# Optimization experiments

Hardware: AMD Instinct MI355X
Metric: run time of the kernel (lower is better)

Reference implementation:

```python
import jax, jax.numpy as jnp
import numpy as np

B, COND_LEN, E = 128, 256, 512   # batch, cond_len, hidden_dim (== conditioning_dim)
A, L, H = 128, 64, 8             # action_dim, num_action_steps, num_heads
STEPS = 20
HD = E // H


def setup_inputs() -> dict:
    key = jax.random.key(0)
    ks = jax.random.split(key, 16)
    def rn(k, shape, s=0.02):
        return jax.random.normal(k, shape, jnp.float32) * s
    return {
        "conditioning": jax.random.normal(ks[0], (B, COND_LEN, E), jnp.float32),
        "noise": jax.random.normal(ks[1], (B, L, A), jnp.float32),
        # time_embed: Linear(1,E) -> ReLU -> Linear(E,E)
        "t1_w": rn(ks[2], (E, 1)), "t1_b": jnp.zeros((E,), jnp.float32),
        "t2_w": rn(ks[3], (E, E)), "t2_b": jnp.zeros((E,), jnp.float32),
        # query_proj: Linear(A, E)
        "qp_w": rn(ks[4], (E, A)), "qp_b": jnp.zeros((E,), jnp.float32),
        # MultiheadAttention packed in_proj (3E, E) and out_proj (E, E)
        "in_w": rn(ks[5], (3 * E, E)), "in_b": jnp.zeros((3 * E,), jnp.float32),
        "op_w": rn(ks[6], (E, E)), "op_b": jnp.zeros((E,), jnp.float32),
        # output_proj: Linear(E, A)
        "outp_w": rn(ks[7], (A, E)), "outp_b": jnp.zeros((A,), jnp.float32),
        # ffn: Linear(A, 4A) -> ReLU -> Linear(4A, A)
        "f1_w": rn(ks[8], (4 * A, A)), "f1_b": jnp.zeros((4 * A,), jnp.float32),
        "f2_w": rn(ks[9], (A, 4 * A)), "f2_b": jnp.zeros((A,), jnp.float32),
        # LayerNorm(A)
        "ln_g": jnp.ones((A,), jnp.float32), "ln_b": jnp.zeros((A,), jnp.float32),
    }


def reference(conditioning, noise, t1_w, t1_b, t2_w, t2_b, qp_w, qp_b,
              in_w, in_b, op_w, op_b, outp_w, outp_b,
              f1_w, f1_b, f2_w, f2_b, ln_g, ln_b):
    dt = -1.0 / STEPS
    scale = 1.0 / np.sqrt(HD)
    # K/V of cross-attn depend only on conditioning -> hoist out of the loop
    # (same math as recomputing per step).
    k = (conditioning @ in_w[E:2 * E].T + in_b[E:2 * E]).reshape(B, COND_LEN, H, HD)
    v = (conditioning @ in_w[2 * E:].T + in_b[2 * E:]).reshape(B, COND_LEN, H, HD)

    def denoise(x_t, time):
        t = time[:, None]                                            # (B,1)
        t_emb = jnp.maximum(t @ t1_w.T + t1_b, 0.0) @ t2_w.T + t2_b  # (B,E)
        q_in = x_t @ qp_w.T + qp_b + t_emb[:, None, :]               # (B,L,E)
        q = (q_in @ in_w[:E].T + in_b[:E]).reshape(B, L, H, HD)
        scores = jnp.einsum('bqhd,bkhd->bhqk', q * scale, k)         # (B,H,L,COND_LEN)
        attn = jax.nn.softmax(scores, axis=-1)
        ctx = jnp.einsum('bhqk,bkhd->bqhd', attn, v).reshape(B, L, E)
        ctx = ctx @ op_w.T + op_b                                    # MHA out_proj
        v_t = ctx @ outp_w.T + outp_b                                # (B,L,A)
        h = x_t + v_t
        mu = jnp.mean(h, axis=-1, keepdims=True)
        var = jnp.mean((h - mu) ** 2, axis=-1, keepdims=True)
        hn = (h - mu) / jnp.sqrt(var + 1e-5) * ln_g + ln_b
        return hn + (jnp.maximum(hn @ f1_w.T + f1_b, 0.0) @ f2_w.T + f2_b)

    def step(carry, _):
        x_t, time = carry
        v_t = denoise(x_t, time)
        return (x_t + dt * v_t, time + dt), None

    init = (noise, jnp.ones((B,), jnp.float32))
    (x_t, _), _ = jax.lax.scan(step, init, None, length=STEPS)
    return x_t
```

## Files before the change

### kernel.cpp

```cpp
#include <hip/hip_runtime.h>

#define NB 128
#define CL 256
#define EE 512
#define AA 128
#define LL 64
#define HH 8
#define HD 64
#define NSTEPS 20
#define BLROWS (NB*LL)
#define LOG2E 1.4426950408889634f
#define QSCALE 64.0f
#define INV_QS 0.015625f

typedef __attribute__((ext_vector_type(8))) short bf16x8;
typedef __attribute__((ext_vector_type(4))) float f32x4;
typedef unsigned int u32;

union F8 { u32 u[2]; long l; };

__device__ __forceinline__ unsigned short f2bf(float f) {
    union { float f; unsigned u; } x; x.f = f;
    unsigned u = x.u;
    u += 0x7fffu + ((u >> 16) & 1u);
    return (unsigned short)(u >> 16);
}
__device__ __forceinline__ u32 pk4f8(f32x4 v) {
    u32 r = __builtin_amdgcn_cvt_pk_fp8_f32(v[0], v[1], 0, false);
    r = __builtin_amdgcn_cvt_pk_fp8_f32(v[2], v[3], r, true);
    return r;
}
__device__ __forceinline__ unsigned char f2f8(float v) {
    return (unsigned char)(__builtin_amdgcn_cvt_pk_fp8_f32(v, v, 0, false) & 0xffu);
}

__device__ __forceinline__ void async_copy16(const unsigned short* g, unsigned short* l) {
    __builtin_amdgcn_global_load_lds((const __attribute__((address_space(1))) u32*)g,
                                     (__attribute__((address_space(3))) u32*)l, 16, 0, 0);
}

#define MFMA(a,b,c)  __builtin_amdgcn_mfma_f32_16x16x32_bf16(a, b, c, 0, 0, 0)
#define MFMA8(a,b,c) __builtin_amdgcn_mfma_f32_16x16x32_fp8_fp8(a, b, c, 0, 0, 0)

__device__ __forceinline__ F8 build8(const u32* p, int kk, int srcA, int srcB, int odd) {
    u32 a0 = __shfl((int)p[2*kk],   srcA, 64);
    u32 b0 = __shfl((int)p[2*kk+1], srcA, 64);
    u32 a1 = __shfl((int)p[2*kk],   srcB, 64);
    u32 b1 = __shfl((int)p[2*kk+1], srcB, 64);
    F8 f; f.u[0] = odd ? b0 : a0; f.u[1] = odd ? b1 : a1;
    return f;
}

__device__ __forceinline__ float softmax8v(const f32x4* sacc, u32* pp8) {
    float mx0 = sacc[0][0], mx1 = sacc[0][1], mx2 = sacc[0][2], mx3 = sacc[0][3];
#pragma unroll
    for (int t = 1; t < 16; ++t) {
        mx0 = fmaxf(mx0, sacc[t][0]);
        mx1 = fmaxf(mx1, sacc[t][1]);
        mx2 = fmaxf(mx2, sacc[t][2]);
        mx3 = fmaxf(mx3, sacc[t][3]);
    }
    float mx = fmaxf(fmaxf(mx0, mx1), fmaxf(mx2, mx3));
    mx = fmaxf(mx, __shfl_xor(mx, 16));
    mx = fmaxf(mx, __shfl_xor(mx, 32));
    float mxc = mx * INV_QS;
    float s0 = 0.f, s1 = 0.f, s2 = 0.f, s3 = 0.f;
#pragma unroll
    for (int t = 0; t < 16; ++t) {
        float e0 = exp2f(fmaf(sacc[t][0], INV_QS, -mxc));
        float e1 = exp2f(fmaf(sacc[t][1], INV_QS, -mxc));
        float e2 = exp2f(fmaf(sacc[t][2], INV_QS, -mxc));
        float e3 = exp2f(fmaf(sacc[t][3], INV_QS, -mxc));
        s0 += e0; s1 += e1; s2 += e2; s3 += e3;
        f32x4 w;
        w[0] = e0 * QSCALE; w[1] = e1 * QSCALE;
        w[2] = e2 * QSCALE; w[3] = e3 * QSCALE;
        pp8[t] = pk4f8(w);
    }
    float sum = (s0 + s1) + (s2 + s3);
    sum += __shfl_xor(sum, 16);
    sum += __shfl_xor(sum, 32);
    return 1.0f / sum;
}


__global__ void cvt8_kernel(const float* __restrict__ src, unsigned short* __restrict__ dst, int n8) {
    int i = blockIdx.x*256 + threadIdx.x;
    if (i >= n8) return;
    const float* s = src + (size_t)i*8;
    f32x4 v0 = *(const f32x4*)s;
    f32x4 v1 = *(const f32x4*)(s + 4);
    bf16x8 o;
    o[0]=(short)f2bf(v0[0]); o[1]=(short)f2bf(v0[1]);
    o[2]=(short)f2bf(v0[2]); o[3]=(short)f2bf(v0[3]);
    o[4]=(short)f2bf(v1[0]); o[5]=(short)f2bf(v1[1]);
    o[6]=(short)f2bf(v1[2]); o[7]=(short)f2bf(v1[3]);
    *(bf16x8*)(dst + (size_t)i*8) = o;
}

__global__ void prep_eff_kernel(const float* __restrict__ in_w, const float* __restrict__ qp_w,
                                const float* __restrict__ outp_w, const float* __restrict__ op_w,
                                const float* __restrict__ op_b, const float* __restrict__ outp_b,
                                unsigned short* __restrict__ wq, unsigned short* __restrict__ wo,
                                float* __restrict__ bo) {
    int tid = blockIdx.x*256 + threadIdx.x;
    if (tid < 65536) {
        int n = tid >> 7, k = tid & 127;
        float s = 0.f;
        for (int e = 0; e < 512; ++e) s += in_w[(size_t)n*512 + e] * qp_w[(size_t)e*128 + k];
        wq[(size_t)n*128 + k] = f2bf(s * (0.125f * LOG2E * QSCALE));
    } else if (tid < 131072) {
        int t2 = tid - 65536; int n = t2 >> 9, k = t2 & 511;
        float s = 0.f;
        for (int e = 0; e < 512; ++e) s += outp_w[(size_t)n*512 + e] * op_w[(size_t)e*512 + k];
        wo[(size_t)n*512 + k] = f2bf(s);
    } else if (tid < 131200) {
        int n = tid - 131072;
        float s = outp_b[n];
        for (int e = 0; e < 512; ++e) s += outp_w[(size_t)n*512 + e] * op_b[e];
        bo[n] = s;
    }
}

__global__ void temb_kernel(const float* __restrict__ t1_w, const float* __restrict__ t1_b,
                            const float* __restrict__ t2_w, const float* __restrict__ t2_b,
                            float* __restrict__ temb) {
    int tid = blockIdx.x*256 + threadIdx.x;
    if (tid >= NSTEPS*512) return;
    int s = tid >> 9, e = tid & 511;
    float t = 1.0f - 0.05f * (float)s;
    float acc = t2_b[e];
    for (int i = 0; i < 512; ++i)
        acc += t2_w[(size_t)e*512 + i] * fmaxf(t * t1_w[i] + t1_b[i], 0.f);
    temb[tid] = acc;
}

__global__ void qbias_kernel(const float* __restrict__ in_w, const float* __restrict__ in_b,
                             const float* __restrict__ qp_b, const float* __restrict__ temb,
                             float* __restrict__ qbias) {
    int tid = blockIdx.x*256 + threadIdx.x;
    if (tid >= NSTEPS*512) return;
    int s = tid >> 9, n = tid & 511;
    float acc = in_b[n];
    const float* te = temb + (size_t)s*512;
    for (int e = 0; e < 512; ++e)
        acc += in_w[(size_t)n*512 + e] * (qp_b[e] + te[e]);
    qbias[tid] = acc * (0.125f * LOG2E * QSCALE);
}

__global__ __launch_bounds__(512, 8) void kv_kernel(const unsigned short* __restrict__ condb,
                                                    const unsigned short* __restrict__ wkv,
                                                    const float* __restrict__ bias,
                                                    unsigned char* __restrict__ K8,
                                                    unsigned char* __restrict__ V8) {
    __shared__ unsigned short As[128*64];
    __shared__ unsigned short Bs[128*64];
    int tid = threadIdx.x;
    int blk = blockIdx.x;
    int xcd = blk & 7, j = blk >> 3;
    int m0 = (xcd*32 + (j >> 3)) * 128;
    int n0 = (j & 7) * 128;
    int wv = tid >> 6, lane = tid & 63, r = lane & 15, q = lane >> 4;
    int srow = lane >> 3;
    int sg = (lane & 7) ^ srow;
    const unsigned short* agl = condb + (size_t)(m0 + wv*16 + srow)*512 + sg*8;
    const unsigned short* bgl = wkv   + (size_t)(n0 + wv*16 + srow)*512 + sg*8;
    f32x4 acc[8] = {};
#pragma unroll
    for (int kt = 0; kt < 8; ++kt) {
        int k0 = kt * 64;
#pragma unroll
        for (int ii = 0; ii < 2; ++ii) {
            async_copy16(agl + (size_t)(ii*8)*512 + k0, &As[(wv*16 + ii*8)*64]);
            async_copy16(bgl + (size_t)(ii*8)*512 + k0, &Bs[(wv*16 + ii*8)*64]);
        }
        __syncthreads();
#pragma unroll
        for (int kk = 0; kk < 2; ++kk) {
            int gof = ((kk*4 + q) ^ (r & 7)) * 8;
            bf16x8 a = *(const bf16x8*)&As[(wv*16 + r)*64 + gof];
#pragma unroll
            for (int t = 0; t < 8; ++t) {
                bf16x8 b = *(const bf16x8*)&Bs[(t*16 + r)*64 + gof];
                acc[t] = MFMA(a, b, acc[t]);
            }
        }
        __syncthreads();
    }
    int mbase = m0 + wv*16 + q*4;
    int bb = mbase >> 8, kpb = mbase & 255;
#pragma unroll
    for (int t = 0; t < 8; ++t) {
        int n = n0 + t*16 + r;
        float bs = bias[n];
        if (n < 512) {
            int h = n >> 6, d = n & 63;
            int colp = ((d>>3)&3)*16 + ((d>>5)&1)*8 + (d&7);
            unsigned char* kp = K8 + (size_t)(bb*HH + h)*16384 + colp;
#pragma unroll
            for (int i = 0; i < 4; ++i)
                kp[(kpb + i)*64] = f2f8(acc[t][i] + bs);
        } else {
            int n2 = n - 512, h = n2 >> 6, d = n2 & 63;
            int kk = kpb >> 5, qq = (kpb >> 3) & 3, jb = kpb & 7;
            int colv = (kk>>1)*64 + qq*16 + (kk&1)*8 + jb;
            u32 w01 = __builtin_amdgcn_cvt_pk_fp8_f32(acc[t][0]+bs, acc[t][1]+bs, 0, false);
            w01 = __builtin_amdgcn_cvt_pk_fp8_f32(acc[t][2]+bs, acc[t][3]+bs, w01, true);
            *(u32*)(V8 + (size_t)(bb*HH + h)*16384 + d*256 + colv) = w01;
        }
    }
}

__global__ __launch_bounds__(512, 2) void mega_kernel(
        const unsigned char* __restrict__ Kg,
        const unsigned char* __restrict__ Vg,
        const float* __restrict__ noise,
        const unsigned short* __restrict__ wq,
        const float* __restrict__ qbiasB,
        const unsigned short* __restrict__ wo,
        const float* __restrict__ bo,
        const float* __restrict__ ln_g, const float* __restrict__ ln_b,
        const unsigned short* __restrict__ f1w,
        const float* __restrict__ f1_b,
        const unsigned short* __restrict__ f2w,
        const float* __restrict__ f2_b,
        float* __restrict__ outp) {
    __shared__ unsigned short xS[32*136];
    __shared__ unsigned short cuS[32*520];
    __shared__ unsigned short hnS[32*136];
    __shared__ float redS[32*4], redS2[32*4];

    int tid = threadIdx.x, w = tid >> 6, lane = tid & 63, r = lane & 15, q = lane >> 4;
    int vblk = ((blockIdx.x & 7) << 5) | (blockIdx.x >> 3);
    int b = vblk >> 1;
    int row0 = vblk * 32;
    int h = w;
    int tB = w & 1, cg = w >> 1;
    int srcA = r + ((2*q) & 3)*16;
    int srcB = r + ((2*q + 1) & 3)*16;
    int odd = (q >> 1) & 1;

    float xf[2][4];
#pragma unroll
    for (int t = 0; t < 2; ++t)
#pragma unroll
        for (int i = 0; i < 4; ++i) {
            int rl = tB*16 + q*4 + i, col = cg*32 + t*16 + r;
            float v = noise[(size_t)(row0 + rl)*AA + col];
            xf[t][i] = v;
            xS[rl*136 + col] = f2bf(v);
        }

    size_t bh = (size_t)b*HH + h;
    const unsigned char* kbase = Kg + bh*16384;
    const unsigned char* vbase = Vg + bh*16384;
    __syncthreads();

    const float dt = -1.f / (float)NSTEPS;

#pragma unroll 1
    for (int s = 0; s < NSTEPS; ++s) {
        const float* qb_s = qbiasB + (size_t)s*512;

        {
            uint4 kbuf[16];
#pragma unroll
            for (int t = 0; t < 16; ++t)
                kbuf[t] = *(const uint4*)(kbase + (size_t)(t*16 + r)*64 + q*16);

            f32x4 qacc0[4] = {}, qacc1[4] = {};
#pragma unroll
            for (int kk = 0; kk < 4; ++kk) {
                bf16x8 bx0 = *(const bf16x8*)&xS[(r)*136 + kk*32 + q*8];
                bf16x8 bx1 = *(const bf16x8*)&xS[(16 + r)*136 + kk*32 + q*8];
#pragma unroll
                for (int t = 0; t < 4; ++t) {
                    bf16x8 a = *(const bf16x8*)(wq + (size_t)(h*HD + t*16 + r)*AA + kk*32 + q*8);
                    qacc0[t] = MFMA(a, bx0, qacc0[t]);
                    qacc1[t] = MFMA(a, bx1, qacc1[t]);
                }
            }
            u32 qp0[4], qp1[4];
#pragma unroll
            for (int t = 0; t < 4; ++t) {
                f32x4 qb4 = *(const f32x4*)(qb_s + h*HD + t*16 + q*4);
                f32x4 v0, v1;
#pragma unroll
                for (int i = 0; i < 4; ++i) { v0[i] = qacc0[t][i] + qb4[i]; v1[i] = qacc1[t][i] + qb4[i]; }
                qp0[t] = pk4f8(v0);
                qp1[t] = pk4f8(v1);
            }
            F8 bq0[2], bq1[2];
            bq0[0] = build8(qp0, 0, srcA, srcB, odd);
            bq0[1] = build8(qp0, 1, srcA, srcB, odd);
            bq1[0] = build8(qp1, 0, srcA, srcB, odd);
            bq1[1] = build8(qp1, 1, srcA, srcB, odd);

            f32x4 s0[16] = {}, s1[16] = {};
#pragma unroll
            for (int t = 0; t < 16; ++t) {
                F8 k0, k1;
                k0.u[0] = kbuf[t].x; k0.u[1] = kbuf[t].y;
                k1.u[0] = kbuf[t].z; k1.u[1] = kbuf[t].w;
                s0[t] = MFMA8(k0.l, bq0[0].l, s0[t]);
                s0[t] = MFMA8(k1.l, bq0[1].l, s0[t]);
                s1[t] = MFMA8(k0.l, bq1[0].l, s1[t]);
                s1[t] = MFMA8(k1.l, bq1[1].l, s1[t]);
            }

            uint4 vbuf[16];
#pragma unroll
            for (int kp = 0; kp < 4; ++kp)
#pragma unroll
                for (int t = 0; t < 4; ++t)
                    vbuf[kp*4 + t] = *(const uint4*)(vbase + (size_t)(t*16 + r)*256 + kp*64 + q*16);

            u32 pp0[16], pp1[16];
            float iv0 = softmax8v(s0, pp0);
            float iv1 = softmax8v(s1, pp1);

            f32x4 c0[4] = {}, c1[4] = {};
#pragma unroll
            for (int kp = 0; kp < 4; ++kp) {
                F8 a00 = build8(pp0, 2*kp,   srcA, srcB, odd);
                F8 a01 = build8(pp0, 2*kp+1, srcA, srcB, odd);
                F8 a10 = build8(pp1, 2*kp,   srcA, srcB, odd);
                F8 a11 = build8(pp1, 2*kp+1, srcA, srcB, odd);
#pragma unroll
                for (int t = 0; t < 4; ++t) {
                    F8 v0, v1;
                    v0.u[0] = vbuf[kp*4+t].x; v0.u[1] = vbuf[kp*4+t].y;
                    v1.u[0] = vbuf[kp*4+t].z; v1.u[1] = vbuf[kp*4+t].w;
                    c0[t] = MFMA8(a00.l, v0.l, c0[t]);
                    c0[t] = MFMA8(a01.l, v1.l, c0[t]);
                    c1[t] = MFMA8(a10.l, v0.l, c1[t]);
                    c1[t] = MFMA8(a11.l, v1.l, c1[t]);
                }
            }
            float sc0[4], sc1[4];
#pragma unroll
            for (int i = 0; i < 4; ++i) {
                sc0[i] = INV_QS * __shfl(iv0, q*4 + i);
                sc1[i] = INV_QS * __shfl(iv1, q*4 + i);
            }
#pragma unroll
            for (int t = 0; t < 4; ++t)
#pragma unroll
                for (int i = 0; i < 4; ++i) {
                    cuS[(q*4 + i)*520 + h*HD + t*16 + r]      = f2bf(c0[t][i] * sc0[i]);
                    cuS[(16 + q*4 + i)*520 + h*HD + t*16 + r] = f2bf(c1[t][i] * sc1[i]);
                }
        }
        __syncthreads();

        f32x4 oacc[2] = {};
#pragma unroll
        for (int kk = 0; kk < 16; ++kk) {
            bf16x8 a = *(const bf16x8*)&cuS[(tB*16 + r)*520 + kk*32 + q*8];
#pragma unroll
            for (int t = 0; t < 2; ++t) {
                bf16x8 bw = *(const bf16x8*)(wo + (size_t)(cg*32 + t*16 + r)*EE + kk*32 + q*8);
                oacc[t] = MFMA(a, bw, oacc[t]);
            }
        }
        float hv[2][4];
#pragma unroll
        for (int t = 0; t < 2; ++t) {
            float bov = bo[cg*32 + t*16 + r];
#pragma unroll
            for (int i = 0; i < 4; ++i) hv[t][i] = oacc[t][i] + bov + xf[t][i];
        }
#pragma unroll
        for (int i = 0; i < 4; ++i) {
            float s1 = hv[0][i] + hv[1][i];
            float s2 = hv[0][i]*hv[0][i] + hv[1][i]*hv[1][i];
            s1 += __shfl_xor(s1, 1);  s2 += __shfl_xor(s2, 1);
            s1 += __shfl_xor(s1, 2);  s2 += __shfl_xor(s2, 2);
            s1 += __shfl_xor(s1, 4);  s2 += __shfl_xor(s2, 4);
            s1 += __shfl_xor(s1, 8);  s2 += __shfl_xor(s2, 8);
            if (r == 0) { redS[(tB*16 + q*4 + i)*4 + cg] = s1; redS2[(tB*16 + q*4 + i)*4 + cg] = s2; }
        }
        __syncthreads();
        float hnv[2][4];
#pragma unroll
        for (int i = 0; i < 4; ++i) {
            int row = tB*16 + q*4 + i;
            float s1 = redS [row*4+0] + redS [row*4+1] + redS [row*4+2] + redS [row*4+3];
            float s2 = redS2[row*4+0] + redS2[row*4+1] + redS2[row*4+2] + redS2[row*4+3];
            float mu = s1 * (1.f/128.f);
            float var = s2 * (1.f/128.f) - mu*mu;
            float rstd = rsqrtf(var + 1e-5f);
#pragma unroll
            for (int t = 0; t < 2; ++t) {
                int col = cg*32 + t*16 + r;
                float v = (hv[t][i] - mu) * rstd * ln_g[col] + ln_b[col];
                hnv[t][i] = v;
                hnS[row*136 + col] = f2bf(v);
            }
        }
        __syncthreads();

        f32x4 o2[2] = {};
#pragma unroll 1
        for (int nt = 0; nt < 4; ++nt) {
            f32x4 a1[2] = {};
#pragma unroll
            for (int kk = 0; kk < 4; ++kk) {
                bf16x8 a = *(const bf16x8*)&hnS[(tB*16 + r)*136 + kk*32 + q*8];
#pragma unroll
                for (int t = 0; t < 2; ++t) {
                    bf16x8 bw = *(const bf16x8*)(f1w + (size_t)(nt*128 + cg*32 + t*16 + r)*AA + kk*32 + q*8);
                    a1[t] = MFMA(a, bw, a1[t]);
                }
            }
#pragma unroll
            for (int t = 0; t < 2; ++t) {
                float b1 = f1_b[nt*128 + cg*32 + t*16 + r];
#pragma unroll
                for (int i = 0; i < 4; ++i)
                    cuS[(tB*16 + q*4 + i)*520 + nt*128 + cg*32 + t*16 + r] = f2bf(fmaxf(a1[t][i] + b1, 0.f));
            }
        }
        __syncthreads();
#pragma unroll 1
        for (int nt = 0; nt < 4; ++nt) {
#pragma unroll
            for (int kk = 0; kk < 4; ++kk) {
                bf16x8 a = *(const bf16x8*)&cuS[(tB*16 + r)*520 + nt*128 + kk*32 + q*8];
#pragma unroll
                for (int t = 0; t < 2; ++t) {
                    bf16x8 bw = *(const bf16x8*)(f2w + (size_t)(cg*32 + t*16 + r)*EE + nt*128 + kk*32 + q*8);
                    o2[t] = MFMA(a, bw, o2[t]);
                }
            }
        }

        if (s < NSTEPS - 1) {
#pragma unroll
            for (int t = 0; t < 2; ++t) {
                float b2 = f2_b[cg*32 + t*16 + r];
#pragma unroll
                for (int i = 0; i < 4; ++i) {
                    float outv = hnv[t][i] + o2[t][i] + b2;
                    float xn = xf[t][i] + dt * outv;
                    xf[t][i] = xn;
                    xS[(tB*16 + q*4 + i)*136 + cg*32 + t*16 + r] = f2bf(xn);
                }
            }
            __syncthreads();
        } else {
#pragma unroll
            for (int t = 0; t < 2; ++t) {
                float b2 = f2_b[cg*32 + t*16 + r];
#pragma unroll
                for (int i = 0; i < 4; ++i) {
                    float outv = hnv[t][i] + o2[t][i] + b2;
                    outp[(size_t)(row0 + tB*16 + q*4 + i)*AA + cg*32 + t*16 + r] = xf[t][i] + dt * outv;
                }
            }
        }
    }
}

extern "C" void kernel_launch(void* const* d_in, const int* in_sizes, int n_in,
                              void* d_out, int out_size, void* d_ws, size_t ws_size,
                              hipStream_t stream) {
    const float* cond   = (const float*)d_in[0];
    const float* noise  = (const float*)d_in[1];
    const float* t1_w   = (const float*)d_in[2];
    const float* t1_b   = (const float*)d_in[3];
    const float* t2_w   = (const float*)d_in[4];
    const float* t2_b   = (const float*)d_in[5];
    const float* qp_w   = (const float*)d_in[6];
    const float* qp_b   = (const float*)d_in[7];
    const float* in_w   = (const float*)d_in[8];
    const float* in_b   = (const float*)d_in[9];
    const float* op_w   = (const float*)d_in[10];
    const float* op_b   = (const float*)d_in[11];
    const float* outp_w = (const float*)d_in[12];
    const float* outp_b = (const float*)d_in[13];
    const float* f1_w   = (const float*)d_in[14];
    const float* f1_b   = (const float*)d_in[15];
    const float* f2_w   = (const float*)d_in[16];
    const float* f2_b   = (const float*)d_in[17];
    const float* ln_g   = (const float*)d_in[18];
    const float* ln_bp  = (const float*)d_in[19];

    char* w = (char*)d_ws;
    auto alloc = [&](size_t bytes) {
        char* p = w;
        w += (bytes + 255) & ~(size_t)255;
        return p;
    };
    unsigned char*  K8     = (unsigned char*)alloc((size_t)NB*HH*CL*HD);
    unsigned char*  V8     = (unsigned char*)alloc((size_t)NB*HH*HD*CL);
    unsigned short* condb  = (unsigned short*)alloc((size_t)NB*CL*EE*2);
    unsigned short* wkv_bf = (unsigned short*)alloc((size_t)1024*512*2);
    unsigned short* wq_bf  = (unsigned short*)alloc((size_t)512*128*2);
    unsigned short* wo_bf  = (unsigned short*)alloc((size_t)128*512*2);
    unsigned short* f1_bf  = (unsigned short*)alloc((size_t)512*128*2);
    unsigned short* f2_bf  = (unsigned short*)alloc((size_t)128*512*2);
    float*          bo_eff = (float*)alloc(128*4);
    float*          tembB  = (float*)alloc((size_t)NSTEPS*512*4);
    float*          qbiasB = (float*)alloc((size_t)NSTEPS*512*4);
    (void)ws_size; (void)n_in; (void)in_sizes; (void)out_size;

    cvt8_kernel<<<8192, 256, 0, stream>>>(cond, condb, NB*CL*EE/8);
    cvt8_kernel<<<256, 256, 0, stream>>>(in_w + 512*512, wkv_bf, 1024*512/8);
    cvt8_kernel<<<32, 256, 0, stream>>>(f1_w, f1_bf, 512*128/8);
    cvt8_kernel<<<32, 256, 0, stream>>>(f2_w, f2_bf, 128*512/8);
    prep_eff_kernel<<<513, 256, 0, stream>>>(in_w, qp_w, outp_w, op_w, op_b, outp_b,
                                             wq_bf, wo_bf, bo_eff);
    temb_kernel<<<40, 256, 0, stream>>>(t1_w, t1_b, t2_w, t2_b, tembB);
    qbias_kernel<<<40, 256, 0, stream>>>(in_w, in_b, qp_b, tembB, qbiasB);
    kv_kernel<<<2048, 512, 0, stream>>>(condb, wkv_bf, in_b + 512, K8, V8);

    mega_kernel<<<256, 512, 0, stream>>>(K8, V8, noise, wq_bf, qbiasB,
                                         wo_bf, bo_eff, ln_g, ln_bp,
                                         f1_bf, f1_b, f2_bf, f2_b,
                                         (float*)d_out);
}
```

Before: 1.369 ms.

## Split attention over key halves with online softmax to cut register pressure

Replaces the single-pass softmax over all 256 keys with a two-chunk online-softmax (flash-style) loop, loading half of K and V per chunk. Running max and sum are rescaled between chunks and the context accumulators are rescaled before each chunk's PV MFMAs. The aim is to halve the live K/V buffers and score accumulators, easing VGPR pressure and possibly raising occupancy or avoiding spills. In exchange it adds rescaling exps, shuffles and multiplies, and puts a serial dependency between the two chunks.

```diff
diff --git a/kernel.cpp b/kernel.cpp
--- a/kernel.cpp
+++ b/kernel.cpp
@@ -49,38 +49,6 @@
     u32 b1 = __shfl((int)p[2*kk+1], srcB, 64);
     F8 f; f.u[0] = odd ? b0 : a0; f.u[1] = odd ? b1 : a1;
     return f;
-}
-
-__device__ __forceinline__ float softmax8v(const f32x4* sacc, u32* pp8) {
-    float mx0 = sacc[0][0], mx1 = sacc[0][1], mx2 = sacc[0][2], mx3 = sacc[0][3];
-#pragma unroll
-    for (int t = 1; t < 16; ++t) {
-        mx0 = fmaxf(mx0, sacc[t][0]);
-        mx1 = fmaxf(mx1, sacc[t][1]);
-        mx2 = fmaxf(mx2, sacc[t][2]);
-        mx3 = fmaxf(mx3, sacc[t][3]);
-    }
-    float mx = fmaxf(fmaxf(mx0, mx1), fmaxf(mx2, mx3));
-    mx = fmaxf(mx, __shfl_xor(mx, 16));
-    mx = fmaxf(mx, __shfl_xor(mx, 32));
-    float mxc = mx * INV_QS;
-    float s0 = 0.f, s1 = 0.f, s2 = 0.f, s3 = 0.f;
-#pragma unroll
-    for (int t = 0; t < 16; ++t) {
-        float e0 = exp2f(fmaf(sacc[t][0], INV_QS, -mxc));
-        float e1 = exp2f(fmaf(sacc[t][1], INV_QS, -mxc));
-        float e2 = exp2f(fmaf(sacc[t][2], INV_QS, -mxc));
-        float e3 = exp2f(fmaf(sacc[t][3], INV_QS, -mxc));
-        s0 += e0; s1 += e1; s2 += e2; s3 += e3;
-        f32x4 w;
-        w[0] = e0 * QSCALE; w[1] = e1 * QSCALE;
-        w[2] = e2 * QSCALE; w[3] = e3 * QSCALE;
-        pp8[t] = pk4f8(w);
-    }
-    float sum = (s0 + s1) + (s2 + s3);
-    sum += __shfl_xor(sum, 16);
-    sum += __shfl_xor(sum, 32);
-    return 1.0f / sum;
 }
 
 
@@ -263,11 +231,6 @@
         const float* qb_s = qbiasB + (size_t)s*512;
 
         {
-            uint4 kbuf[16];
-#pragma unroll
-            for (int t = 0; t < 16; ++t)
-                kbuf[t] = *(const uint4*)(kbase + (size_t)(t*16 + r)*64 + q*16);
-
             f32x4 qacc0[4] = {}, qacc1[4] = {};
 #pragma unroll
             for (int kk = 0; kk < 4; ++kk) {
@@ -296,47 +259,115 @@
             bq1[0] = build8(qp1, 0, srcA, srcB, odd);
             bq1[1] = build8(qp1, 1, srcA, srcB, odd);
 
-            f32x4 s0[16] = {}, s1[16] = {};
-#pragma unroll
-            for (int t = 0; t < 16; ++t) {
-                F8 k0, k1;
-                k0.u[0] = kbuf[t].x; k0.u[1] = kbuf[t].y;
-                k1.u[0] = kbuf[t].z; k1.u[1] = kbuf[t].w;
-                s0[t] = MFMA8(k0.l, bq0[0].l, s0[t]);
-                s0[t] = MFMA8(k1.l, bq0[1].l, s0[t]);
-                s1[t] = MFMA8(k0.l, bq1[0].l, s1[t]);
-                s1[t] = MFMA8(k1.l, bq1[1].l, s1[t]);
-            }
-
-            uint4 vbuf[16];
-#pragma unroll
-            for (int kp = 0; kp < 4; ++kp)
+            float m0r = -3e38f, m1r = -3e38f;
+            float l0 = 0.f, l1 = 0.f;
+            f32x4 c0[4] = {}, c1[4] = {};
+
+#pragma unroll
+            for (int hh = 0; hh < 2; ++hh) {
+                uint4 kbuf[8];
+#pragma unroll
+                for (int t = 0; t < 8; ++t)
+                    kbuf[t] = *(const uint4*)(kbase + (size_t)((hh*8 + t)*16 + r)*64 + q*16);
+
+                f32x4 s0[8] = {}, s1[8] = {};
+#pragma unroll
+                for (int t = 0; t < 8; ++t) {
+                    F8 k0, k1;
+                    k0.u[0] = kbuf[t].x; k0.u[1] = kbuf[t].y;
+                    k1.u[0] = kbuf[t].z; k1.u[1] = kbuf[t].w;
+                    s0[t] = MFMA8(k0.l, bq0[0].l, s0[t]);
+                    s0[t] = MFMA8(k1.l, bq0[1].l, s0[t]);
+                    s1[t] = MFMA8(k0.l, bq1[0].l, s1[t]);
+                    s1[t] = MFMA8(k1.l, bq1[1].l, s1[t]);
+                }
+
+                uint4 vbuf[8];
+#pragma unroll
+                for (int kp = 0; kp < 2; ++kp)
+#pragma unroll
+                    for (int t = 0; t < 4; ++t)
+                        vbuf[kp*4 + t] = *(const uint4*)(vbase + (size_t)(t*16 + r)*256 + (hh*2 + kp)*64 + q*16);
+
+                float a0 = s0[0][0], a1 = s0[0][1], a2 = s0[0][2], a3 = s0[0][3];
+                float b0 = s1[0][0], b1 = s1[0][1], b2 = s1[0][2], b3 = s1[0][3];
+#pragma unroll
+                for (int t = 1; t < 8; ++t) {
+                    a0 = fmaxf(a0, s0[t][0]); a1 = fmaxf(a1, s0[t][1]);
+                    a2 = fmaxf(a2, s0[t][2]); a3 = fmaxf(a3, s0[t][3]);
+                    b0 = fmaxf(b0, s1[t][0]); b1 = fmaxf(b1, s1[t][1]);
+                    b2 = fmaxf(b2, s1[t][2]); b3 = fmaxf(b3, s1[t][3]);
+                }
+                float hm0 = fmaxf(fmaxf(a0, a1), fmaxf(a2, a3));
+                float hm1 = fmaxf(fmaxf(b0, b1), fmaxf(b2, b3));
+                hm0 = fmaxf(hm0, __shfl_xor(hm0, 16));
+                hm0 = fmaxf(hm0, __shfl_xor(hm0, 32));
+                hm1 = fmaxf(hm1, __shfl_xor(hm1, 16));
+                hm1 = fmaxf(hm1, __shfl_xor(hm1, 32));
+                float nm0 = fmaxf(m0r, hm0 * INV_QS);
+                float nm1 = fmaxf(m1r, hm1 * INV_QS);
+                float rs0 = exp2f(m0r - nm0);
+                float rs1 = exp2f(m1r - nm1);
+                m0r = nm0; m1r = nm1;
+
+                u32 pp0[8], pp1[8];
+                float t00 = 0.f, t01 = 0.f, t10 = 0.f, t11 = 0.f;
+#pragma unroll
+                for (int t = 0; t < 8; ++t) {
+                    float e0 = exp2f(fmaf(s0[t][0], INV_QS, -nm0));
+                    float e1 = exp2f(fmaf(s0[t][1], INV_QS, -nm0));
+                    float e2 = exp2f(fmaf(s0[t][2], INV_QS, -nm0));
+                    float e3 = exp2f(fmaf(s0[t][3], INV_QS, -nm0));
+                    t00 += e0 + e2; t01 += e1 + e3;
+                    f32x4 w0; w0[0]=e0*QSCALE; w0[1]=e1*QSCALE; w0[2]=e2*QSCALE; w0[3]=e3*QSCALE;
+                    pp0[t] = pk4f8(w0);
+                    float f0 = exp2f(fmaf(s1[t][0], INV_QS, -nm1));
+                    float f1 = exp2f(fmaf(s1[t][1], INV_QS, -nm1));
+                    float f2 = exp2f(fmaf(s1[t][2], INV_QS, -nm1));
+                    float f3 = exp2f(fmaf(s1[t][3], INV_QS, -nm1));
+                    t10 += f0 + f2; t11 += f1 + f3;
+                    f32x4 w1; w1[0]=f0*QSCALE; w1[1]=f1*QSCALE; w1[2]=f2*QSCALE; w1[3]=f3*QSCALE;
+                    pp1[t] = pk4f8(w1);
+                }
+                l0 = l0 * rs0 + (t00 + t01);
+                l1 = l1 * rs1 + (t10 + t11);
+
+                float rr0[4], rr1[4];
+#pragma unroll
+                for (int i = 0; i < 4; ++i) {
+                    rr0[i] = __shfl(rs0, q*4 + i);
+                    rr1[i] = __shfl(rs1, q*4 + i);
+                }
 #pragma unroll
                 for (int t = 0; t < 4; ++t)
-                    vbuf[kp*4 + t] = *(const uint4*)(vbase + (size_t)(t*16 + r)*256 + kp*64 + q*16);
-
-            u32 pp0[16], pp1[16];
-            float iv0 = softmax8v(s0, pp0);
-            float iv1 = softmax8v(s1, pp1);
-
-            f32x4 c0[4] = {}, c1[4] = {};
-#pragma unroll
-            for (int kp = 0; kp < 4; ++kp) {
-                F8 a00 = build8(pp0, 2*kp,   srcA, srcB, odd);
-                F8 a01 = build8(pp0, 2*kp+1, srcA, srcB, odd);
-                F8 a10 = build8(pp1, 2*kp,   srcA, srcB, odd);
-                F8 a11 = build8(pp1, 2*kp+1, srcA, srcB, odd);
-#pragma unroll
-                for (int t = 0; t < 4; ++t) {
-                    F8 v0, v1;
-                    v0.u[0] = vbuf[kp*4+t].x; v0.u[1] = vbuf[kp*4+t].y;
-                    v1.u[0] = vbuf[kp*4+t].z; v1.u[1] = vbuf[kp*4+t].w;
-                    c0[t] = MFMA8(a00.l, v0.l, c0[t]);
-                    c0[t] = MFMA8(a01.l, v1.l, c0[t]);
-                    c1[t] = MFMA8(a10.l, v0.l, c1[t]);
-                    c1[t] = MFMA8(a11.l, v1.l, c1[t]);
-                }
-            }
+#pragma unroll
+                    for (int i = 0; i < 4; ++i) {
+                        c0[t][i] *= rr0[i];
+                        c1[t][i] *= rr1[i];
+                    }
+
+#pragma unroll
+                for (int kp = 0; kp < 2; ++kp) {
+                    F8 a00 = build8(pp0, 2*kp,   srcA, srcB, odd);
+                    F8 a01 = build8(pp0, 2*kp+1, srcA, srcB, odd);
+                    F8 a10 = build8(pp1, 2*kp,   srcA, srcB, odd);
+                    F8 a11 = build8(pp1, 2*kp+1, srcA, srcB, odd);
+#pragma unroll
+                    for (int t = 0; t < 4; ++t) {
+                        F8 v0, v1;
+                        v0.u[0] = vbuf[kp*4+t].x; v0.u[1] = vbuf[kp*4+t].y;
+                        v1.u[0] = vbuf[kp*4+t].z; v1.u[1] = vbuf[kp*4+t].w;
+                        c0[t] = MFMA8(a00.l, v0.l, c0[t]);
+                        c0[t] = MFMA8(a01.l, v1.l, c0[t]);
+                        c1[t] = MFMA8(a10.l, v0.l, c1[t]);
+                        c1[t] = MFMA8(a11.l, v1.l, c1[t]);
+                    }
+                }
+            }
+
+            l0 += __shfl_xor(l0, 16); l0 += __shfl_xor(l0, 32);
+            l1 += __shfl_xor(l1, 16); l1 += __shfl_xor(l1, 32);
+            float iv0 = 1.0f / l0, iv1 = 1.0f / l1;
             float sc0[4], sc1[4];
 #pragma unroll
             for (int i = 0; i < 4; ++i) {
```

After: 1.312 ms. 1.04x faster.
